# Kernel tuning notes

Measured on AMD Instinct MI355X. Metric: run time of the kernel, lower is better.

The kernel has to match this reference:

```python
import jax, jax.numpy as jnp
import numpy as np

SP, WD, H, HID = 8, 3, 8, 256
D = HID // H
TEMP = 0.1


def setup_inputs() -> dict:
    key = jax.random.key(0)
    ks = jax.random.split(key, 14)
    B, Lq, Lk, F = 4, 1024, 2048, SP + WD
    s = 0.05
    return {
        "q_fp": jax.random.normal(ks[0], (B, Lq, F), jnp.float32),
        "v_ret": jax.random.normal(ks[1], (B, Lk, F), jnp.float32),
        "pi_star": jax.random.uniform(ks[2], (B, Lq, Lk), jnp.float32),
        "Wq_s": jax.random.normal(ks[3], (HID, SP), jnp.float32) * s,
        "bq_s": jax.random.normal(ks[4], (HID,), jnp.float32) * s,
        "Wk_s": jax.random.normal(ks[5], (HID, SP), jnp.float32) * s,
        "bk_s": jax.random.normal(ks[6], (HID,), jnp.float32) * s,
        "Wq_w": jax.random.normal(ks[7], (HID, WD), jnp.float32) * s,
        "bq_w": jax.random.normal(ks[8], (HID,), jnp.float32) * s,
        "Wk_w": jax.random.normal(ks[9], (HID, WD), jnp.float32) * s,
        "bk_w": jax.random.normal(ks[10], (HID,), jnp.float32) * s,
        "Wv": jax.random.normal(ks[11], (HID, F), jnp.float32) * s,
        "bv": jnp.zeros((HID,), jnp.float32),
        "Wo": jax.random.normal(ks[12], (HID, HID), jnp.float32) * s,
        "bo": jnp.zeros((HID,), jnp.float32),
        "wave_blend": jnp.array(0.5, jnp.float32),
    }


def _proj(x, W, b):
    # x: [B, L, F_in] -> [B, H, L, D]
    B, L, _ = x.shape
    return (x @ W.T + b).reshape(B, L, H, D).transpose(0, 2, 1, 3)


def reference(q_fp, v_ret, pi_star, Wq_s, bq_s, Wk_s, bk_s, Wq_w, bq_w, Wk_w, bk_w, Wv, bv, Wo, bo, wave_blend):
    B, Lq, _ = q_fp.shape
    # split streams: first SP dims spatial, next WD dims wave (F == SP+WD)
    q_sp, q_wv = q_fp[..., :SP], q_fp[..., SP:SP + WD]
    k_sp, k_wv = v_ret[..., :SP], v_ret[..., SP:SP + WD]
    # structural branch: scaled dot product
    q_struct = _proj(q_sp, Wq_s, bq_s)
    k_struct = _proj(k_sp, Wk_s, bk_s)
    spatial_logits = jnp.einsum('bhqd,bhkd->bhqk', q_struct, k_struct) / np.float32(np.sqrt(D))
    # wave branch: negative squared euclidean distance via norm expansion
    q_wp = _proj(q_wv, Wq_w, bq_w)
    k_wp = _proj(k_wv, Wk_w, bk_w)
    qn = jnp.sum(q_wp * q_wp, axis=-1)[..., :, None]   # [B,H,Lq,1]
    kn = jnp.sum(k_wp * k_wp, axis=-1)[..., None, :]   # [B,H,1,Lk]
    qk = jnp.einsum('bhqd,bhkd->bhqk', q_wp, k_wp)
    wave_logits = -(qn + kn - 2.0 * qk) / np.float32(TEMP)
    alpha = jax.nn.sigmoid(wave_blend)
    transport_mask = jnp.log(jnp.clip(pi_star, 1e-9, None))[:, None]  # [B,1,Lq,Lk]
    attn = jax.nn.softmax((1.0 - alpha) * spatial_logits + alpha * wave_logits + transport_mask, axis=-1)
    values = _proj(v_ret, Wv, bv)  # [B,H,Lk,D]
    ctx = jnp.einsum('bhqk,bhkd->bhqd', attn, values)
    ctx = ctx.transpose(0, 2, 1, 3).reshape(B, Lq, HID)
    return ctx @ Wo.T + bo
```

## Files before the change

### kernel.cpp

```cpp
#include <hip/hip_runtime.h>
#include <hip/hip_bf16.h>
#include <cstdint>

#define B_    4
#define LQ    1024
#define LK    2048
#define FEAT  11
#define SP_   8
#define WD_   3
#define H_    8
#define HID_  256
#define LOG2E 1.4426950408889634f
#define SPLIT 2
#define KPS   (LK / SPLIT)
#define ITERS (KPS / 64)

typedef __attribute__((ext_vector_type(4))) float f32x4;
typedef __attribute__((ext_vector_type(8))) short bf16x8;

__device__ __forceinline__ float sigmoidf_(float x) { return 1.f / (1.f + __expf(-x)); }

__device__ __forceinline__ short f2bf(float f) {
  unsigned u = __float_as_uint(f);
  u += 0x7fffu + ((u >> 16) & 1u);
  return (short)(u >> 16);
}

__device__ __forceinline__ void gl_lds16(const void* g, void* l) {
  __builtin_amdgcn_global_load_lds(
      (const __attribute__((address_space(1))) unsigned int*)g,
      (__attribute__((address_space(3))) unsigned int*)l, 16, 0, 0);
}

__global__ __launch_bounds__(256) void proj_q_kernel(
    const float* __restrict__ q_fp, const float* __restrict__ Wq_s,
    const float* __restrict__ bq_s, const float* __restrict__ Wq_w,
    const float* __restrict__ bq_w, const float* __restrict__ wb,
    short* __restrict__ Qh)
{
  const int row = blockIdx.x;
  const int t   = threadIdx.x;
  const float alpha = sigmoidf_(wb[0]);
  const float c1 = (1.f - alpha) * 0.17677669529663687f * LOG2E;
  const float c2 = 2.f * alpha * 10.f * LOG2E;

  const float* x = q_fp + (size_t)row * FEAT;
  float xs[FEAT];
  #pragma unroll
  for (int f = 0; f < FEAT; ++f) xs[f] = x[f];

  float s = bq_s[t];
  #pragma unroll
  for (int f = 0; f < SP_; ++f) s += xs[f] * Wq_s[t * SP_ + f];
  float w = bq_w[t];
  #pragma unroll
  for (int f = 0; f < WD_; ++f) w += xs[SP_ + f] * Wq_w[t * WD_ + f];

  const int h = t >> 5, d = t & 31;
  const int b = row >> 10, q = row & (LQ - 1);
  const size_t base = ((size_t)(b * H_ + h) * LQ + q) * 64;
  Qh[base + d]      = f2bf(c1 * s);
  Qh[base + 32 + d] = f2bf(c2 * w);
}

__global__ __launch_bounds__(256) void proj_k_kernel(
    const float* __restrict__ v_ret, const float* __restrict__ Wk_s,
    const float* __restrict__ bk_s, const float* __restrict__ Wk_w,
    const float* __restrict__ bk_w, const float* __restrict__ Wv,
    const float* __restrict__ bv,   const float* __restrict__ wb,
    short* __restrict__ Kh, float* __restrict__ Vp, float* __restrict__ kb)
{
  const int row = blockIdx.x;
  const int t   = threadIdx.x;
  const float alpha = sigmoidf_(wb[0]);

  const float* x = v_ret + (size_t)row * FEAT;
  float xs[FEAT];
  #pragma unroll
  for (int f = 0; f < FEAT; ++f) xs[f] = x[f];

  float s = bk_s[t];
  #pragma unroll
  for (int f = 0; f < SP_; ++f) s += xs[f] * Wk_s[t * SP_ + f];
  float w = bk_w[t];
  #pragma unroll
  for (int f = 0; f < WD_; ++f) w += xs[SP_ + f] * Wk_w[t * WD_ + f];
  float v = bv[t];
  #pragma unroll
  for (int f = 0; f < FEAT; ++f) v += xs[f] * Wv[t * FEAT + f];

  const int h = t >> 5, d = t & 31;
  const int b = row >> 11, k = row & (LK - 1);
  const size_t kcb = (size_t)(b * H_ + h) * LK + k;
  Kh[kcb * 64 + d]      = f2bf(s);
  Kh[kcb * 64 + 32 + d] = f2bf(w);
  Vp[kcb * 32 + d]      = v;

  float sq = w * w;
  #pragma unroll
  for (int off = 16; off >= 1; off >>= 1) sq += __shfl_down(sq, off, 32);
  if (d == 0) kb[kcb] = -10.f * alpha * LOG2E * sq;
}

__global__ __launch_bounds__(256) void prepack_kernel(
    const short* __restrict__ Kh, const float* __restrict__ Vp,
    short* __restrict__ KV)
{
  __shared__ float ldsv[64][33];
  const int blk = blockIdx.x, bh = blockIdx.y;
  const int t = threadIdx.x;

  {
    const int row = t >> 2, part = t & 3;
    const float* src = Vp + ((size_t)bh * LK + blk * 64 + row) * 32 + part * 8;
    f32x4 a = *(const f32x4*)(src);
    f32x4 b = *(const f32x4*)(src + 4);
    #pragma unroll
    for (int i = 0; i < 4; ++i) { ldsv[row][part * 8 + i] = a[i]; ldsv[row][part * 8 + 4 + i] = b[i]; }
  }

  const size_t base = ((size_t)bh * 32 + blk) * 768;
  #pragma unroll
  for (int gs = 0; gs < 2; ++gs) {
    const int g = gs * 256 + t;
    const int j = g >> 6, lane = g & 63;
    const int t4 = j >> 1, half = j & 1;
    const int quad = lane >> 4, lo = lane & 15;
    const int off = ((t4 >> 1) << 5) + ((t4 & 1) << 2);
    const int kk = blk * 64 + off + ((lo >> 2) << 3) + (lo & 3);
    bf16x8 v = *(const bf16x8*)(Kh + ((size_t)bh * LK + kk) * 64 + quad * 8 + half * 32);
    *(bf16x8*)(KV + (base + g) * 8) = v;
  }

  __syncthreads();

  {
    const int g = t;
    const int j = g >> 6, lane = g & 63;
    const int dt = j >> 1, kw = j & 1;
    const int quad = lane >> 4, lo = lane & 15;
    bf16x8 hv;
    #pragma unroll
    for (int i = 0; i < 8; ++i)
      hv[i] = f2bf(ldsv[kw * 32 + quad * 8 + i][dt * 16 + lo]);
    *(bf16x8*)(KV + (base + 512 + g) * 8) = hv;
  }
}

union PF { int i[4]; bf16x8 v; };

__global__ __launch_bounds__(256, 4) void attn_kernel(
    const short* __restrict__ Qh, const short* __restrict__ KV,
    const float* __restrict__ kb, const float* __restrict__ pi,
    float* __restrict__ part)
{
  __shared__ short skv[2][6144];
  const int bh = blockIdx.y;
  const int sp = blockIdx.z;
  const int b = bh >> 3;
  const int wv = threadIdx.x >> 6;
  const int lane = threadIdx.x & 63;
  const int lo16 = lane & 15;
  const int quad = lane >> 4;
  const int q = blockIdx.x * 64 + wv * 16 + lo16;
  const int k0 = sp * KPS;
  const int blk0 = sp * 16;

  const size_t qoff = ((size_t)bh * LQ + q) * 64 + quad * 8;
  const bf16x8 qh0 = *(const bf16x8*)(Qh + qoff);
  const bf16x8 qh1 = *(const bf16x8*)(Qh + qoff + 32);

  const float* pibase = pi + ((size_t)b * LQ + q) * LK + k0 + quad * 8;
  const float* kbbase = kb + (size_t)bh * LK + k0 + quad * 8;

  float m = -1e30f, l = 0.f;
  f32x4 o0 = {0.f, 0.f, 0.f, 0.f}, o1 = {0.f, 0.f, 0.f, 0.f};

  {
    const size_t gb = ((size_t)bh * 32 + blk0) * 768;
    #pragma unroll
    for (int c = 0; c < 3; ++c)
      gl_lds16(KV + (gb + c * 256 + wv * 64 + lane) * 8,
               &skv[0][c * 2048 + wv * 512]);
  }

  #pragma unroll 2
  for (int it = 0; it < ITERS; ++it) {
    __syncthreads();
    if (it + 1 < ITERS) {
      const size_t gb = ((size_t)bh * 32 + blk0 + it + 1) * 768;
      short* db = skv[(it + 1) & 1];
      #pragma unroll
      for (int c = 0; c < 3; ++c)
        gl_lds16(KV + (gb + c * 256 + wv * 64 + lane) * 8,
                 db + c * 2048 + wv * 512);
    }
    const short* cbuf = skv[it & 1];

    const float* pp = pibase + it * 64;
    const float* bp = kbbase + it * 64;
    f32x4 pi4[4], kb4[4];
    pi4[0] = *(const f32x4*)(pp);      pi4[1] = *(const f32x4*)(pp + 4);
    pi4[2] = *(const f32x4*)(pp + 32); pi4[3] = *(const f32x4*)(pp + 36);
    kb4[0] = *(const f32x4*)(bp);      kb4[1] = *(const f32x4*)(bp + 4);
    kb4[2] = *(const f32x4*)(bp + 32); kb4[3] = *(const f32x4*)(bp + 36);

    f32x4 st[4];
    #pragma unroll
    for (int t4 = 0; t4 < 4; ++t4) {
      const bf16x8 ka0 = *(const bf16x8*)(cbuf + ((t4 * 2 + 0) * 64 + lane) * 8);
      const bf16x8 ka1 = *(const bf16x8*)(cbuf + ((t4 * 2 + 1) * 64 + lane) * 8);
      f32x4 z = {0.f, 0.f, 0.f, 0.f};
      z = __builtin_amdgcn_mfma_f32_16x16x32_bf16(ka0, qh0, z, 0, 0, 0);
      z = __builtin_amdgcn_mfma_f32_16x16x32_bf16(ka1, qh1, z, 0, 0, 0);
      st[t4] = z;
    }

    float lg[16];
    #pragma unroll
    for (int t4 = 0; t4 < 4; ++t4) {
      #pragma unroll
      for (int r = 0; r < 4; ++r) lg[t4 * 4 + r] = st[t4][r] + kb4[t4][r];
    }

    float cm = lg[0];
    #pragma unroll
    for (int j = 1; j < 16; ++j) cm = fmaxf(cm, lg[j]);
    cm = fmaxf(cm, __shfl_xor(cm, 16));
    cm = fmaxf(cm, __shfl_xor(cm, 32));
    const float mn = fmaxf(m, cm);
    const float sc = __builtin_amdgcn_exp2f(m - mn);

    unsigned eu[16];
    #pragma unroll
    for (int t4 = 0; t4 < 4; ++t4) {
      #pragma unroll
      for (int r = 0; r < 4; ++r)
        eu[t4 * 4 + r] = __float_as_uint(
            __builtin_amdgcn_exp2f(lg[t4 * 4 + r] - mn) * fmaxf(pi4[t4][r], 1e-9f));
    }

    PF pf0, pf1;
    float ps = 0.f;
    #pragma unroll
    for (int p = 0; p < 4; ++p) {
      const int w0 = __builtin_amdgcn_perm(eu[2 * p + 1], eu[2 * p], 0x07060302u);
      const int w1 = __builtin_amdgcn_perm(eu[8 + 2 * p + 1], eu[8 + 2 * p], 0x07060302u);
      pf0.i[p] = w0; pf1.i[p] = w1;
      ps += __uint_as_float(((unsigned)w0) << 16) + __uint_as_float(w0 & 0xffff0000u);
      ps += __uint_as_float(((unsigned)w1) << 16) + __uint_as_float(w1 & 0xffff0000u);
    }
    ps += __shfl_xor(ps, 16);
    ps += __shfl_xor(ps, 32);
    l = l * sc + ps;
    m = mn;
    #pragma unroll
    for (int r = 0; r < 4; ++r) { o0[r] *= sc; o1[r] *= sc; }

    const bf16x8 va00 = *(const bf16x8*)(cbuf + ((512 + 0 * 64) + lane) * 8);
    const bf16x8 va01 = *(const bf16x8*)(cbuf + ((512 + 1 * 64) + lane) * 8);
    const bf16x8 va10 = *(const bf16x8*)(cbuf + ((512 + 2 * 64) + lane) * 8);
    const bf16x8 va11 = *(const bf16x8*)(cbuf + ((512 + 3 * 64) + lane) * 8);
    o0 = __builtin_amdgcn_mfma_f32_16x16x32_bf16(va00, pf0.v, o0, 0, 0, 0);
    o0 = __builtin_amdgcn_mfma_f32_16x16x32_bf16(va01, pf1.v, o0, 0, 0, 0);
    o1 = __builtin_amdgcn_mfma_f32_16x16x32_bf16(va10, pf0.v, o1, 0, 0, 0);
    o1 = __builtin_amdgcn_mfma_f32_16x16x32_bf16(va11, pf1.v, o1, 0, 0, 0);
  }

  float* ppart = part + ((size_t)(sp * 32 + bh) * LQ + q) * 36;
  if (quad == 0) { ppart[0] = m; ppart[1] = l; }
  *(f32x4*)(ppart + 4 + quad * 4)  = o0;
  *(f32x4*)(ppart + 20 + quad * 4) = o1;
}

__global__ __launch_bounds__(256) void combine_kernel(
    const float* __restrict__ part, float* __restrict__ ctx)
{
  const int g = blockIdx.x * 256 + threadIdx.x;
  const int r = g >> 5;
  const int d = g & 31;
  const int bh = r >> 10, qq = r & (LQ - 1);
  const int b = bh >> 3, h = bh & 7;

  const float* p0 = part + (size_t)r * 36;
  const float* p1 = part + (size_t)(B_ * H_ * LQ + r) * 36;
  const float m0 = p0[0], l0 = p0[1], m1 = p1[0], l1 = p1[1];
  const float mM = fmaxf(m0, m1);
  const float w0 = __builtin_amdgcn_exp2f(m0 - mM);
  const float w1 = __builtin_amdgcn_exp2f(m1 - mM);
  const float num = w0 * p0[4 + d] + w1 * p1[4 + d];
  const float den = w0 * l0 + w1 * l1;
  ctx[((size_t)(b * LQ + qq)) * HID_ + h * 32 + d] = num / den;
}

__global__ __launch_bounds__(256) void out_kernel(
    const float* __restrict__ ctx, const float* __restrict__ Wo,
    const float* __restrict__ bo, float* __restrict__ out)
{
  __shared__ float cs[16 * 256];
  const int t = threadIdx.x;
  const size_t r0 = (size_t)blockIdx.x * 16;

  const f32x4* src = reinterpret_cast<const f32x4*>(ctx + r0 * HID_);
  f32x4* dst = reinterpret_cast<f32x4*>(cs);
  #pragma unroll
  for (int i = 0; i < 4; ++i) dst[i * 256 + t] = src[i * 256 + t];
  __syncthreads();

  const int o0 = (t & 63) * 4;
  const int rs = (t >> 6) * 4;
  float acc[4][4];
  #pragma unroll
  for (int r = 0; r < 4; ++r) {
    #pragma unroll
    for (int j = 0; j < 4; ++j) acc[r][j] = bo[o0 + j];
  }

  for (int c4 = 0; c4 < 64; ++c4) {
    const f32x4 w0 = *(const f32x4*)(Wo + (size_t)(o0 + 0) * HID_ + c4 * 4);
    const f32x4 w1 = *(const f32x4*)(Wo + (size_t)(o0 + 1) * HID_ + c4 * 4);
    const f32x4 w2 = *(const f32x4*)(Wo + (size_t)(o0 + 2) * HID_ + c4 * 4);
    const f32x4 w3 = *(const f32x4*)(Wo + (size_t)(o0 + 3) * HID_ + c4 * 4);
    #pragma unroll
    for (int r = 0; r < 4; ++r) {
      const f32x4 cv = *(const f32x4*)(cs + (rs + r) * 256 + c4 * 4);
      acc[r][0] += cv[0] * w0[0] + cv[1] * w0[1] + cv[2] * w0[2] + cv[3] * w0[3];
      acc[r][1] += cv[0] * w1[0] + cv[1] * w1[1] + cv[2] * w1[2] + cv[3] * w1[3];
      acc[r][2] += cv[0] * w2[0] + cv[1] * w2[1] + cv[2] * w2[2] + cv[3] * w2[3];
      acc[r][3] += cv[0] * w3[0] + cv[1] * w3[1] + cv[2] * w3[2] + cv[3] * w3[3];
    }
  }
  #pragma unroll
  for (int r = 0; r < 4; ++r) {
    f32x4 res;
    res[0] = acc[r][0]; res[1] = acc[r][1]; res[2] = acc[r][2]; res[3] = acc[r][3];
    *(f32x4*)(out + (r0 + rs + r) * HID_ + o0) = res;
  }
}

extern "C" void kernel_launch(void* const* d_in, const int* in_sizes, int n_in,
                              void* d_out, int out_size, void* d_ws, size_t ws_size,
                              hipStream_t stream)
{
  const float* q_fp  = (const float*)d_in[0];
  const float* v_ret = (const float*)d_in[1];
  const float* pi    = (const float*)d_in[2];
  const float* Wq_s  = (const float*)d_in[3];
  const float* bq_s  = (const float*)d_in[4];
  const float* Wk_s  = (const float*)d_in[5];
  const float* bk_s  = (const float*)d_in[6];
  const float* Wq_w  = (const float*)d_in[7];
  const float* bq_w  = (const float*)d_in[8];
  const float* Wk_w  = (const float*)d_in[9];
  const float* bk_w  = (const float*)d_in[10];
  const float* Wv    = (const float*)d_in[11];
  const float* bv    = (const float*)d_in[12];
  const float* Wo    = (const float*)d_in[13];
  const float* bo    = (const float*)d_in[14];
  const float* wb    = (const float*)d_in[15];
  float* out = (float*)d_out;

  short* Qh   = (short*)d_ws;
  short* KV   = Qh + (size_t)2097152;
  float* kbuf = (float*)(KV + (size_t)6291456);
  float* ctx  = kbuf + (size_t)65536;
  short* Kh   = (short*)(ctx + (size_t)1048576);
  float* Vp   = (float*)(Kh + (size_t)4194304);
  float* part = (float*)Kh;

  proj_q_kernel<<<B_ * LQ, 256, 0, stream>>>(q_fp, Wq_s, bq_s, Wq_w, bq_w, wb, Qh);
  proj_k_kernel<<<B_ * LK, 256, 0, stream>>>(v_ret, Wk_s, bk_s, Wk_w, bk_w, Wv, bv, wb,
                                             Kh, Vp, kbuf);
  prepack_kernel<<<dim3(LK / 64, 32), 256, 0, stream>>>(Kh, Vp, KV);
  attn_kernel<<<dim3(LQ / 64, 32, SPLIT), 256, 0, stream>>>(Qh, KV, kbuf, pi, part);
  combine_kernel<<<(B_ * H_ * LQ * 32) / 256, 256, 0, stream>>>(part, ctx);
  out_kernel<<<(B_ * LQ) / 16, 256, 0, stream>>>(ctx, Wo, bo, out);
}
```

Baseline: 215.5 us.

## Fuse K projection with prepack, fuse combine into output GEMM, prepack pi

Merges the K/V projection into the prepack kernel so the intermediate Kh/Vp buffers are never written or reread. The split-K combine is folded into the output projection's LDS staging, which drops the ctx buffer and one launch. A new kernel rewrites pi_star into a per-lane contiguous tile layout so the attention kernel's pi loads are fully coalesced. The catch is that the pi prepack reads and writes all of pi (32 MB) once more, which may cost more than the better coalescing saves.

```diff
diff --git a/kernel.cpp b/kernel.cpp
--- a/kernel.cpp
+++ b/kernel.cpp
@@ -63,95 +63,99 @@
   Qh[base + 32 + d] = f2bf(c2 * w);
 }
 
-__global__ __launch_bounds__(256) void proj_k_kernel(
+__global__ __launch_bounds__(256) void projk_pack_kernel(
     const float* __restrict__ v_ret, const float* __restrict__ Wk_s,
     const float* __restrict__ bk_s, const float* __restrict__ Wk_w,
     const float* __restrict__ bk_w, const float* __restrict__ Wv,
     const float* __restrict__ bv,   const float* __restrict__ wb,
-    short* __restrict__ Kh, float* __restrict__ Vp, float* __restrict__ kb)
-{
-  const int row = blockIdx.x;
-  const int t   = threadIdx.x;
-  const float alpha = sigmoidf_(wb[0]);
-
-  const float* x = v_ret + (size_t)row * FEAT;
-  float xs[FEAT];
-  #pragma unroll
-  for (int f = 0; f < FEAT; ++f) xs[f] = x[f];
-
-  float s = bk_s[t];
-  #pragma unroll
-  for (int f = 0; f < SP_; ++f) s += xs[f] * Wk_s[t * SP_ + f];
-  float w = bk_w[t];
-  #pragma unroll
-  for (int f = 0; f < WD_; ++f) w += xs[SP_ + f] * Wk_w[t * WD_ + f];
-  float v = bv[t];
-  #pragma unroll
-  for (int f = 0; f < FEAT; ++f) v += xs[f] * Wv[t * FEAT + f];
-
-  const int h = t >> 5, d = t & 31;
-  const int b = row >> 11, k = row & (LK - 1);
-  const size_t kcb = (size_t)(b * H_ + h) * LK + k;
-  Kh[kcb * 64 + d]      = f2bf(s);
-  Kh[kcb * 64 + 32 + d] = f2bf(w);
-  Vp[kcb * 32 + d]      = v;
-
-  float sq = w * w;
-  #pragma unroll
-  for (int off = 16; off >= 1; off >>= 1) sq += __shfl_down(sq, off, 32);
-  if (d == 0) kb[kcb] = -10.f * alpha * LOG2E * sq;
-}
-
-__global__ __launch_bounds__(256) void prepack_kernel(
-    const short* __restrict__ Kh, const float* __restrict__ Vp,
-    short* __restrict__ KV)
+    short* __restrict__ KV, float* __restrict__ kb)
 {
   __shared__ float ldsv[64][33];
   const int blk = blockIdx.x, bh = blockIdx.y;
+  const int b = bh >> 3, h = bh & 7;
   const int t = threadIdx.x;
+  const int kl = t >> 2, part = t & 3;
+  const int k = blk * 64 + kl;
+  const float alpha = sigmoidf_(wb[0]);
+
+  const float* x = v_ret + (size_t)(b * LK + k) * FEAT;
+  float xs[FEAT];
+  #pragma unroll
+  for (int f = 0; f < FEAT; ++f) xs[f] = x[f];
+
+  float s8[8], w8[8], v8[8];
+  #pragma unroll
+  for (int i = 0; i < 8; ++i) {
+    const int d = h * 32 + part * 8 + i;
+    float s = bk_s[d];
+    #pragma unroll
+    for (int f = 0; f < SP_; ++f) s += xs[f] * Wk_s[d * SP_ + f];
+    float w = bk_w[d];
+    #pragma unroll
+    for (int f = 0; f < WD_; ++f) w += xs[SP_ + f] * Wk_w[d * WD_ + f];
+    float v = bv[d];
+    #pragma unroll
+    for (int f = 0; f < FEAT; ++f) v += xs[f] * Wv[d * FEAT + f];
+    s8[i] = s; w8[i] = w; v8[i] = v;
+    ldsv[kl][part * 8 + i] = v;
+  }
+
+  float sq = 0.f;
+  #pragma unroll
+  for (int i = 0; i < 8; ++i) sq += w8[i] * w8[i];
+  sq += __shfl_xor(sq, 1);
+  sq += __shfl_xor(sq, 2);
+  if (part == 0) kb[(size_t)bh * LK + k] = -10.f * alpha * LOG2E * sq;
+
+  const int a  = kl >> 5;
+  const int bb = (kl >> 2) & 1;
+  const int p  = kl - a * 32 - bb * 4;
+  const int lo = ((p >> 3) << 2) | (p & 3);
+  const int t4 = a * 2 + bb;
+  const size_t base = ((size_t)bh * 32 + blk) * 768;
+
+  bf16x8 hs, hw;
+  #pragma unroll
+  for (int i = 0; i < 8; ++i) { hs[i] = f2bf(s8[i]); hw[i] = f2bf(w8[i]); }
+  *(bf16x8*)(KV + (base + (t4 * 2 + 0) * 64 + part * 16 + lo) * 8) = hs;
+  *(bf16x8*)(KV + (base + (t4 * 2 + 1) * 64 + part * 16 + lo) * 8) = hw;
+
+  __syncthreads();
 
   {
-    const int row = t >> 2, part = t & 3;
-    const float* src = Vp + ((size_t)bh * LK + blk * 64 + row) * 32 + part * 8;
-    f32x4 a = *(const f32x4*)(src);
-    f32x4 b = *(const f32x4*)(src + 4);
-    #pragma unroll
-    for (int i = 0; i < 4; ++i) { ldsv[row][part * 8 + i] = a[i]; ldsv[row][part * 8 + 4 + i] = b[i]; }
-  }
-
-  const size_t base = ((size_t)bh * 32 + blk) * 768;
-  #pragma unroll
-  for (int gs = 0; gs < 2; ++gs) {
-    const int g = gs * 256 + t;
-    const int j = g >> 6, lane = g & 63;
-    const int t4 = j >> 1, half = j & 1;
-    const int quad = lane >> 4, lo = lane & 15;
-    const int off = ((t4 >> 1) << 5) + ((t4 & 1) << 2);
-    const int kk = blk * 64 + off + ((lo >> 2) << 3) + (lo & 3);
-    bf16x8 v = *(const bf16x8*)(Kh + ((size_t)bh * LK + kk) * 64 + quad * 8 + half * 32);
-    *(bf16x8*)(KV + (base + g) * 8) = v;
-  }
-
-  __syncthreads();
-
-  {
-    const int g = t;
-    const int j = g >> 6, lane = g & 63;
+    const int j = t >> 6, l = t & 63;
     const int dt = j >> 1, kw = j & 1;
-    const int quad = lane >> 4, lo = lane & 15;
+    const int lo2 = l & 15, quad = l >> 4;
+    const int d = dt * 16 + lo2;
     bf16x8 hv;
     #pragma unroll
     for (int i = 0; i < 8; ++i)
-      hv[i] = f2bf(ldsv[kw * 32 + quad * 8 + i][dt * 16 + lo]);
-    *(bf16x8*)(KV + (base + 512 + g) * 8) = hv;
-  }
+      hv[i] = f2bf(ldsv[kw * 32 + quad * 8 + i][d]);
+    *(bf16x8*)(KV + (base + 512 + t) * 8) = hv;
+  }
+}
+
+__global__ __launch_bounds__(256) void pi_prepack_kernel(
+    const float* __restrict__ pi, float* __restrict__ piP)
+{
+  const int Gid = blockIdx.x * 256 + threadIdx.x;
+  const int g    = Gid & 255;
+  const int kblk = (Gid >> 8) & 31;
+  const int qt   = (Gid >> 13) & 63;
+  const int b    = Gid >> 19;
+  const int t4 = g >> 6, l = g & 63;
+  const int lo = l & 15, quad = l >> 4;
+  const int q = qt * 16 + lo;
+  const int k = kblk * 64 + ((t4 >> 1) << 5) + ((t4 & 1) << 2) + quad * 8;
+  const f32x4 v = *(const f32x4*)(pi + ((size_t)(b * LQ + q) * LK + k));
+  *(f32x4*)(piP + (size_t)Gid * 4) = v;
 }
 
 union PF { int i[4]; bf16x8 v; };
 
 __global__ __launch_bounds__(256, 4) void attn_kernel(
     const short* __restrict__ Qh, const short* __restrict__ KV,
-    const float* __restrict__ kb, const float* __restrict__ pi,
+    const float* __restrict__ kb, const float* __restrict__ piP,
     float* __restrict__ part)
 {
   __shared__ short skv[2][6144];
@@ -163,6 +167,7 @@
   const int lo16 = lane & 15;
   const int quad = lane >> 4;
   const int q = blockIdx.x * 64 + wv * 16 + lo16;
+  const int qt = blockIdx.x * 4 + wv;
   const int k0 = sp * KPS;
   const int blk0 = sp * 16;
 
@@ -170,7 +175,7 @@
   const bf16x8 qh0 = *(const bf16x8*)(Qh + qoff);
   const bf16x8 qh1 = *(const bf16x8*)(Qh + qoff + 32);
 
-  const float* pibase = pi + ((size_t)b * LQ + q) * LK + k0 + quad * 8;
+  const float* pibase = piP + (((size_t)(b * 64 + qt) * 32 + blk0) << 10) + lane * 4;
   const float* kbbase = kb + (size_t)bh * LK + k0 + quad * 8;
 
   float m = -1e30f, l = 0.f;
@@ -197,11 +202,12 @@
     }
     const short* cbuf = skv[it & 1];
 
-    const float* pp = pibase + it * 64;
+    const float* pp = pibase + (it << 10);
+    f32x4 pi4[4];
+    #pragma unroll
+    for (int t4 = 0; t4 < 4; ++t4) pi4[t4] = *(const f32x4*)(pp + t4 * 256);
     const float* bp = kbbase + it * 64;
-    f32x4 pi4[4], kb4[4];
-    pi4[0] = *(const f32x4*)(pp);      pi4[1] = *(const f32x4*)(pp + 4);
-    pi4[2] = *(const f32x4*)(pp + 32); pi4[3] = *(const f32x4*)(pp + 36);
+    f32x4 kb4[4];
     kb4[0] = *(const f32x4*)(bp);      kb4[1] = *(const f32x4*)(bp + 4);
     kb4[2] = *(const f32x4*)(bp + 32); kb4[3] = *(const f32x4*)(bp + 36);
 
@@ -273,38 +279,38 @@
   *(f32x4*)(ppart + 20 + quad * 4) = o1;
 }
 
-__global__ __launch_bounds__(256) void combine_kernel(
-    const float* __restrict__ part, float* __restrict__ ctx)
-{
-  const int g = blockIdx.x * 256 + threadIdx.x;
-  const int r = g >> 5;
-  const int d = g & 31;
-  const int bh = r >> 10, qq = r & (LQ - 1);
-  const int b = bh >> 3, h = bh & 7;
-
-  const float* p0 = part + (size_t)r * 36;
-  const float* p1 = part + (size_t)(B_ * H_ * LQ + r) * 36;
-  const float m0 = p0[0], l0 = p0[1], m1 = p1[0], l1 = p1[1];
-  const float mM = fmaxf(m0, m1);
-  const float w0 = __builtin_amdgcn_exp2f(m0 - mM);
-  const float w1 = __builtin_amdgcn_exp2f(m1 - mM);
-  const float num = w0 * p0[4 + d] + w1 * p1[4 + d];
-  const float den = w0 * l0 + w1 * l1;
-  ctx[((size_t)(b * LQ + qq)) * HID_ + h * 32 + d] = num / den;
-}
-
 __global__ __launch_bounds__(256) void out_kernel(
-    const float* __restrict__ ctx, const float* __restrict__ Wo,
+    const float* __restrict__ part, const float* __restrict__ Wo,
     const float* __restrict__ bo, float* __restrict__ out)
 {
   __shared__ float cs[16 * 256];
   const int t = threadIdx.x;
   const size_t r0 = (size_t)blockIdx.x * 16;
 
-  const f32x4* src = reinterpret_cast<const f32x4*>(ctx + r0 * HID_);
-  f32x4* dst = reinterpret_cast<f32x4*>(cs);
-  #pragma unroll
-  for (int i = 0; i < 4; ++i) dst[i * 256 + t] = src[i * 256 + t];
+  {
+    const int col4 = (t & 63) * 4;
+    const int h = col4 >> 5, d = col4 & 31;
+    #pragma unroll
+    for (int i = 0; i < 4; ++i) {
+      const int row = i * 4 + (t >> 6);
+      const size_t gq = r0 + row;
+      const int b = (int)(gq >> 10), qq = (int)(gq & (LQ - 1));
+      const size_t r = ((size_t)(b * H_ + h) * LQ + qq);
+      const float* p0 = part + r * 36;
+      const float* p1 = part + (r + (size_t)B_ * H_ * LQ) * 36;
+      const float m0 = p0[0], l0 = p0[1], m1 = p1[0], l1 = p1[1];
+      const float mM = fmaxf(m0, m1);
+      const float w0 = __builtin_amdgcn_exp2f(m0 - mM);
+      const float w1 = __builtin_amdgcn_exp2f(m1 - mM);
+      const float inv = 1.f / (w0 * l0 + w1 * l1);
+      const f32x4 a0 = *(const f32x4*)(p0 + 4 + d);
+      const f32x4 a1 = *(const f32x4*)(p1 + 4 + d);
+      f32x4 cv;
+      #pragma unroll
+      for (int j = 0; j < 4; ++j) cv[j] = (w0 * a0[j] + w1 * a1[j]) * inv;
+      *(f32x4*)(cs + row * 256 + col4) = cv;
+    }
+  }
   __syncthreads();
 
   const int o0 = (t & 63) * 4;
@@ -363,16 +369,13 @@
   short* Qh   = (short*)d_ws;
   short* KV   = Qh + (size_t)2097152;
   float* kbuf = (float*)(KV + (size_t)6291456);
-  float* ctx  = kbuf + (size_t)65536;
-  short* Kh   = (short*)(ctx + (size_t)1048576);
-  float* Vp   = (float*)(Kh + (size_t)4194304);
-  float* part = (float*)Kh;
+  float* piP  = kbuf + (size_t)65536;
+  float* part = piP + (size_t)8388608;
 
   proj_q_kernel<<<B_ * LQ, 256, 0, stream>>>(q_fp, Wq_s, bq_s, Wq_w, bq_w, wb, Qh);
-  proj_k_kernel<<<B_ * LK, 256, 0, stream>>>(v_ret, Wk_s, bk_s, Wk_w, bk_w, Wv, bv, wb,
-                                             Kh, Vp, kbuf);
-  prepack_kernel<<<dim3(LK / 64, 32), 256, 0, stream>>>(Kh, Vp, KV);
-  attn_kernel<<<dim3(LQ / 64, 32, SPLIT), 256, 0, stream>>>(Qh, KV, kbuf, pi, part);
-  combine_kernel<<<(B_ * H_ * LQ * 32) / 256, 256, 0, stream>>>(part, ctx);
-  out_kernel<<<(B_ * LQ) / 16, 256, 0, stream>>>(ctx, Wo, bo, out);
-}
+  projk_pack_kernel<<<dim3(LK / 64, 32), 256, 0, stream>>>(
+      v_ret, Wk_s, bk_s, Wk_w, bk_w, Wv, bv, wb, KV, kbuf);
+  pi_prepack_kernel<<<8192, 256, 0, stream>>>(pi, piP);
+  attn_kernel<<<dim3(LQ / 64, 32, SPLIT), 256, 0, stream>>>(Qh, KV, kbuf, piP, part);
+  out_kernel<<<(B_ * LQ) / 16, 256, 0, stream>>>(part, Wo, bo, out);
+}
```

New measurement: 205.2 us. 1.05x faster.
